# Kernel tuning notes

Measured on AMD Instinct MI355X. Metric: run time of the kernel, lower is better.

## Reference

```python
import jax, jax.numpy as jnp
import numpy as np

H = 1024      # hidden_size
F = 1024      # intermediate_size
E = 8         # num_experts
K = 2         # num_experts_per_tok
B, S = 1, 2048


def setup_inputs() -> dict:
    key = jax.random.key(0)
    ks = jax.random.split(key, 8)
    s = 0.02
    return {
        "hidden_states": jax.random.normal(ks[0], (B, S, H), jnp.float32),
        "w_gate": jax.random.normal(ks[1], (H, E), jnp.float32) * s,
        "w_gate_proj": jax.random.normal(ks[2], (E, H, F), jnp.float32) * s,   # per-expert gate_proj
        "w_up_proj": jax.random.normal(ks[3], (E, H, F), jnp.float32) * s,     # per-expert up_proj
        "w_down_proj": jax.random.normal(ks[4], (E, F, H), jnp.float32) * s,   # per-expert down_proj
        "w_shared_gate": jax.random.normal(ks[5], (H, F), jnp.float32) * s,
        "w_shared_up": jax.random.normal(ks[6], (H, F), jnp.float32) * s,
        "w_shared_down": jax.random.normal(ks[7], (F, H), jnp.float32) * s,
    }


def reference(hidden_states, w_gate, w_gate_proj, w_up_proj, w_down_proj,
              w_shared_gate, w_shared_up, w_shared_down):
    b, s, h = hidden_states.shape
    x = hidden_states.reshape(-1, h)                       # [T, H]
    t = x.shape[0]

    # --- router ---
    router_logits = x @ w_gate                             # [T, E]
    topk_vals, topk_idx = jax.lax.top_k(router_logits, K)  # [T, K]
    expert_weights = jax.nn.softmax(topk_vals.astype(jnp.float32), axis=-1).astype(x.dtype)

    # dense per-token per-expert combine weight [T, E] (zero where not selected)
    combine = jnp.zeros((t, E), x.dtype).at[jnp.arange(t)[:, None], topk_idx].add(expert_weights)

    # --- all experts as one grouped GEMM (weight-zero experts contribute 0) ---
    g = jnp.einsum('th,ehf->tef', x, w_gate_proj)          # [T, E, F]
    u = jnp.einsum('th,ehf->tef', x, w_up_proj)            # [T, E, F]
    y = jnp.einsum('tef,efh->teh', jax.nn.silu(g) * u, w_down_proj)  # [T, E, H]
    out = jnp.einsum('teh,te->th', y, combine)             # [T, H]

    # --- shared expert ---
    shared = (jax.nn.silu(x @ w_shared_gate) * (x @ w_shared_up)) @ w_shared_down
    out = (out + shared).reshape(b, s, h)

    aux_loss = jnp.float32(0.0)
    return out, aux_loss
```

## Files before the change

kernel.cpp:

```cpp
#include <hip/hip_runtime.h>
#include <hip/hip_bf16.h>
#include <stdint.h>

#define HDIM 1024
#define FDIM 1024
#define TTOK 2048
#define CAP  2048
#define MSZ  (1024*1024)

typedef __attribute__((ext_vector_type(8))) __bf16 bf16x8;
typedef __attribute__((ext_vector_type(4))) float  f32x4;

static __device__ __forceinline__ unsigned short f2bf(float v) {
  unsigned int u = __float_as_uint(v);
  u += 0x7FFF + ((u >> 16) & 1);
  return (unsigned short)(u >> 16);
}

static __device__ __forceinline__ unsigned pk2(float a, float b) {
  return (unsigned)f2bf(a) | ((unsigned)f2bf(b) << 16);
}

static __device__ __forceinline__ void gload_lds16(const void* g, void* l) {
  __builtin_amdgcn_global_load_lds(
      (const __attribute__((address_space(1))) unsigned int*)g,
      (__attribute__((address_space(3))) unsigned int*)l, 16, 0, 0);
}


__global__ __launch_bounds__(256) void k_trw(
    const float* __restrict__ wgp, const float* __restrict__ wsg,
    const float* __restrict__ wup, const float* __restrict__ wsu,
    const float* __restrict__ wdp, const float* __restrict__ wsd,
    unsigned short* __restrict__ wB) {
  int b = blockIdx.x;
  int tid = threadIdx.x;
  int m = b >> 6;
  int idx = b & 63;
  int rb = (idx >> 3) << 7;
  int cb = (idx & 7) << 7;
  const float* src;
  if (m < 8)       src = wgp + (size_t)m * MSZ;
  else if (m == 8) src = wsg;
  else if (m < 17) src = wup + (size_t)(m - 9) * MSZ;
  else if (m == 17) src = wsu;
  else if (m < 26) src = wdp + (size_t)(m - 18) * MSZ;
  else             src = wsd;
  unsigned short* dst = wB + (size_t)m * MSZ;
  __shared__ __align__(16) unsigned short T[128 * 128];
  #pragma unroll
  for (int i = 0; i < 16; i++) {
    int g = tid + (i << 8);
    int r = g >> 5;
    int f4 = g & 31;
    float4 v = *(const float4*)(src + (size_t)(rb + r) * 1024 + cb + (f4 << 2));
    uint2 p;
    p.x = pk2(v.x, v.y);
    p.y = pk2(v.z, v.w);
    int ps = (f4 + ((r >> 3) << 1)) & 31;
    *(uint2*)(T + r * 128 + (ps << 2)) = p;
  }
  __syncthreads();
  int L = tid & 63, w = tid >> 6;
  int q = L & 15;
  int cbase = (w << 2) + (L >> 4);
  #pragma unroll
  for (int j = 0; j < 8; j++) {
    int c = cbase + (j << 4);
    int ps = ((c >> 2) + (q << 1)) & 31;
    const unsigned short* p = T + (q << 3) * 128 + (ps << 2) + (c & 3);
    unsigned short u0 = p[0],       u1 = p[128],      u2 = p[2 * 128],
                   u3 = p[3 * 128], u4 = p[4 * 128],  u5 = p[5 * 128],
                   u6 = p[6 * 128], u7 = p[7 * 128];
    uint4 o;
    o.x = (unsigned)u0 | ((unsigned)u1 << 16);
    o.y = (unsigned)u2 | ((unsigned)u3 << 16);
    o.z = (unsigned)u4 | ((unsigned)u5 << 16);
    o.w = (unsigned)u6 | ((unsigned)u7 << 16);
    *(uint4*)(dst + (size_t)(cb + c) * 1024 + rb + (q << 3)) = o;
  }
}

__global__ __launch_bounds__(256) void k_rt(
    const float* __restrict__ x, const float* __restrict__ wg,
    unsigned short* __restrict__ xb,
    int* __restrict__ counts, int* __restrict__ tok_id, float* __restrict__ tok_w,
    int2* __restrict__ tsl, float* __restrict__ tw) {
  int b = blockIdx.x;
  int tid = threadIdx.x;
  if (b < 1024) {
    int i = b * 256 + tid;
    const float4* in4 = (const float4*)x;
    float4 f0 = in4[i * 2], f1 = in4[i * 2 + 1];
    uint4 v;
    v.x = pk2(f0.x, f0.y); v.y = pk2(f0.z, f0.w);
    v.z = pk2(f1.x, f1.y); v.w = pk2(f1.z, f1.w);
    *((uint4*)(xb + (size_t)i * 8)) = v;
    if (i < TTOK) { tok_id[8 * CAP + i] = i; tok_w[8 * CAP + i] = 1.0f; }
    if (i == 0) counts[8 << 4] = TTOK;
  } else {
    int t = ((b - 1024) << 2) + (tid >> 6);
    int L = tid & 63;
    const float* xr = x + (size_t)t * HDIM;
    float acc[8] = {0, 0, 0, 0, 0, 0, 0, 0};
    for (int h = L; h < HDIM; h += 64) {
      float xv = xr[h];
      const float* wr = wg + h * 8;
      #pragma unroll
      for (int e = 0; e < 8; e++) acc[e] += xv * wr[e];
    }
    #pragma unroll
    for (int e = 0; e < 8; e++) {
      float v = acc[e];
      for (int off = 32; off > 0; off >>= 1) v += __shfl_xor(v, off);
      acc[e] = v;
    }
    if (L == 0) {
      int i1 = 0; float v1 = acc[0];
      #pragma unroll
      for (int e = 1; e < 8; e++) if (acc[e] > v1) { v1 = acc[e]; i1 = e; }
      int i2 = -1; float v2 = -1e30f;
      #pragma unroll
      for (int e = 0; e < 8; e++) if (e != i1 && acc[e] > v2) { v2 = acc[e]; i2 = e; }
      float ex = __expf(v2 - v1);
      float w1 = 1.f / (1.f + ex);
      float w2 = 1.f - w1;
      int p1 = atomicAdd(&counts[i1 << 4], 1);
      tok_id[i1 * CAP + p1] = t; tok_w[i1 * CAP + p1] = w1;
      int p2 = atomicAdd(&counts[i2 << 4], 1);
      tok_id[i2 * CAP + p2] = t; tok_w[i2 * CAP + p2] = w2;
      tsl[t] = make_int2((i1 << 10) + p1, (i2 << 10) + p2);
      tw[t] = w1;
    }
  }
}


__global__ __launch_bounds__(256, 4) void k_gemm1(
    const unsigned short* __restrict__ xb, const unsigned short* __restrict__ wB,
    const int* __restrict__ counts, const int* __restrict__ tok_id,
    unsigned short* __restrict__ actb) {
  int lin = blockIdx.x;
  int e = lin >> 8;
  int r9 = lin & 255;
  int nbi = (r9 & 7) | ((r9 >> 7) << 3);
  int mi  = (r9 >> 3) & 15;
  int Ne = (e == 8) ? TTOK : counts[e << 4];
  int rb = mi << 7;
  if (rb >= Ne) return;
  int nb = nbi << 6;
  const unsigned short* wg = wB + (size_t)e * MSZ;
  const unsigned short* wu = wB + (size_t)(9 + e) * MSZ;
  __shared__ __align__(16) unsigned short As[128 * 64];
  __shared__ __align__(16) unsigned short Bgs[64 * 64];
  __shared__ __align__(16) unsigned short Bus[64 * 64];
  int tid = threadIdx.x;
  int w = tid >> 6, L = tid & 63;
  int quad = L >> 4, lane15 = L & 15;
  int wr = w >> 1, wc = w & 1;
  int l7 = lane15 & 7;
  int sw8 = ((L & 7) ^ (L >> 3)) << 3;
  const int* tlist = tok_id + e * CAP + rb;
  int trow[4];
  #pragma unroll
  for (int r = 0; r < 4; r++) {
    int row = (w << 5) + (r << 3) + (L >> 3);
    trow[r] = (rb + row < Ne) ? tlist[row] : 0;
  }
  f32x4 accg[4][2], accu[4][2];
  #pragma unroll
  for (int mt = 0; mt < 4; mt++)
    #pragma unroll
    for (int nt = 0; nt < 2; nt++) {
      accg[mt][nt] = (f32x4){0.f, 0.f, 0.f, 0.f};
      accu[mt][nt] = (f32x4){0.f, 0.f, 0.f, 0.f};
    }
  for (int it = 0; it < 16; it++) {
    int k0 = it << 6;
    #pragma unroll
    for (int r = 0; r < 4; r++)
      gload_lds16(xb + (size_t)trow[r] * 1024 + k0 + sw8, As + ((w << 2) + r) * 512);
    #pragma unroll
    for (int r = 0; r < 2; r++) {
      int fr = (((w << 1) + r) << 3) + (L >> 3);
      size_t go = (size_t)(nb + fr) * 1024 + k0 + sw8;
      gload_lds16(wg + go, Bgs + ((w << 1) + r) * 512);
      gload_lds16(wu + go, Bus + ((w << 1) + r) * 512);
    }
    __syncthreads();
    #pragma unroll
    for (int s = 0; s < 2; s++) {
      bf16x8 a[4], bg[2], bu[2];
      int ch = (s << 2) + quad;
      int po = ((ch ^ l7) << 3);
      #pragma unroll
      for (int mt = 0; mt < 4; mt++)
        a[mt] = *(const bf16x8*)(As + (((wr << 6) + (mt << 4) + lane15) << 6) + po);
      #pragma unroll
      for (int nt = 0; nt < 2; nt++) {
        int rrow = ((wc << 5) + (nt << 4) + lane15) << 6;
        bg[nt] = *(const bf16x8*)(Bgs + rrow + po);
        bu[nt] = *(const bf16x8*)(Bus + rrow + po);
      }
      #pragma unroll
      for (int mt = 0; mt < 4; mt++)
        #pragma unroll
        for (int nt = 0; nt < 2; nt++) {
          accg[mt][nt] = __builtin_amdgcn_mfma_f32_16x16x32_bf16(a[mt], bg[nt], accg[mt][nt], 0, 0, 0);
          accu[mt][nt] = __builtin_amdgcn_mfma_f32_16x16x32_bf16(a[mt], bu[nt], accu[mt][nt], 0, 0, 0);
        }
    }
    __syncthreads();
  }
  #pragma unroll
  for (int mt = 0; mt < 4; mt++)
    #pragma unroll
    for (int nt = 0; nt < 2; nt++)
      #pragma unroll
      for (int g = 0; g < 4; g++) {
        int r = (wr << 6) + (mt << 4) + (quad << 2) + g;
        if (rb + r < Ne) {
          float gv = accg[mt][nt][g], uv = accu[mt][nt][g];
          float av = gv / (1.f + __expf(-gv)) * uv;
          int f = nb + (wc << 5) + (nt << 4) + lane15;
          actb[(size_t)(e * CAP + rb + r) * 1024 + f] = f2bf(av);
        }
      }
}

__global__ __launch_bounds__(256, 4) void k_gemm2(
    const unsigned short* __restrict__ actb, const unsigned short* __restrict__ wB,
    const int* __restrict__ counts, float* __restrict__ y) {
  int lin = blockIdx.x;
  int e = lin >> 8;
  int r8 = lin & 255;
  int nbi = r8 & 7;
  int mi  = r8 >> 3;
  int Ne = (e == 8) ? TTOK : counts[e << 4];
  int rb = mi << 6;
  if (rb >= Ne) return;
  int nb = nbi << 7;
  int yb = (e < 8) ? (e << 10) : 8192;
  const unsigned short* wd = wB + (size_t)(18 + e) * MSZ;
  __shared__ __align__(16) unsigned short As[64 * 64];
  __shared__ __align__(16) unsigned short Bs[128 * 64];
  int tid = threadIdx.x;
  int w = tid >> 6, L = tid & 63;
  int quad = L >> 4, lane15 = L & 15;
  int l7 = lane15 & 7;
  int sw8 = ((L & 7) ^ (L >> 3)) << 3;
  const unsigned short* arow = actb + (size_t)(e * CAP + rb) * 1024;
  f32x4 acc[4][2];
  #pragma unroll
  for (int mt = 0; mt < 4; mt++)
    #pragma unroll
    for (int nt = 0; nt < 2; nt++) acc[mt][nt] = (f32x4){0.f, 0.f, 0.f, 0.f};
  for (int it = 0; it < 16; it++) {
    int k0 = it << 6;
    #pragma unroll
    for (int r = 0; r < 2; r++) {
      int row = (w << 4) + (r << 3) + (L >> 3);
      gload_lds16(arow + (size_t)row * 1024 + k0 + sw8, As + ((w << 1) + r) * 512);
    }
    #pragma unroll
    for (int r = 0; r < 4; r++) {
      int row = (w << 5) + (r << 3) + (L >> 3);
      gload_lds16(wd + (size_t)(nb + row) * 1024 + k0 + sw8, Bs + ((w << 2) + r) * 512);
    }
    __syncthreads();
    #pragma unroll
    for (int s = 0; s < 2; s++) {
      bf16x8 a[4], b[2];
      int ch = (s << 2) + quad;
      int po = ((ch ^ l7) << 3);
      #pragma unroll
      for (int mt = 0; mt < 4; mt++)
        a[mt] = *(const bf16x8*)(As + (((mt << 4) + lane15) << 6) + po);
      #pragma unroll
      for (int nt = 0; nt < 2; nt++)
        b[nt] = *(const bf16x8*)(Bs + (((w << 5) + (nt << 4) + lane15) << 6) + po);
      #pragma unroll
      for (int mt = 0; mt < 4; mt++)
        #pragma unroll
        for (int nt = 0; nt < 2; nt++)
          acc[mt][nt] = __builtin_amdgcn_mfma_f32_16x16x32_bf16(a[mt], b[nt], acc[mt][nt], 0, 0, 0);
    }
    __syncthreads();
  }
  #pragma unroll
  for (int mt = 0; mt < 4; mt++)
    #pragma unroll
    for (int nt = 0; nt < 2; nt++)
      #pragma unroll
      for (int g = 0; g < 4; g++) {
        int r = (mt << 4) + (quad << 2) + g;
        if (rb + r < Ne) {
          int hc = nb + (w << 5) + (nt << 4) + lane15;
          y[(size_t)(yb + rb + r) * 1024 + hc] = acc[mt][nt][g];
        }
      }
}

__global__ __launch_bounds__(256) void k_comb(
    const float* __restrict__ y, const int2* __restrict__ tsl,
    const float* __restrict__ tw, float* __restrict__ out) {
  int t = blockIdx.x, tid = threadIdx.x;
  int2 s = tsl[t];
  float w0 = tw[t], w1 = 1.f - w0;
  const float4* y4 = (const float4*)y;
  float4 a = y4[(size_t)s.x * 256 + tid];
  float4 b = y4[(size_t)s.y * 256 + tid];
  float4 c = y4[(size_t)(8192 + t) * 256 + tid];
  float4 o;
  o.x = w0 * a.x + w1 * b.x + c.x;
  o.y = w0 * a.y + w1 * b.y + c.y;
  o.z = w0 * a.z + w1 * b.z + c.z;
  o.w = w0 * a.w + w1 * b.w + c.w;
  ((float4*)out)[(size_t)t * 256 + tid] = o;
}

extern "C" void kernel_launch(void* const* d_in, const int* in_sizes, int n_in,
                              void* d_out, int out_size, void* d_ws, size_t ws_size,
                              hipStream_t stream) {
  (void)in_sizes; (void)n_in; (void)ws_size; (void)out_size;
  const float* x   = (const float*)d_in[0];
  const float* wg  = (const float*)d_in[1];
  const float* wgp = (const float*)d_in[2];
  const float* wup = (const float*)d_in[3];
  const float* wdp = (const float*)d_in[4];
  const float* wsg = (const float*)d_in[5];
  const float* wsu = (const float*)d_in[6];
  const float* wsd = (const float*)d_in[7];
  float* out = (float*)d_out;
  char* ws = (char*)d_ws;
  unsigned short* wB   = (unsigned short*)ws;
  unsigned short* xb   = (unsigned short*)(ws + 56623104);
  unsigned short* actb = (unsigned short*)(ws + 60817408);
  float* y      = (float*)(ws + 98566144);
  int*   tok_id = (int*)(ws + 140509184);
  float* tok_w  = (float*)(ws + 140582912);
  int2*  tsl    = (int2*)(ws + 140656640);
  float* tw     = (float*)(ws + 140673024);
  int*   counts = (int*)(ws + 140681216);

  hipMemsetAsync(counts, 0, 576, stream);
  k_trw<<<1728, 256, 0, stream>>>(wgp, wsg, wup, wsu, wdp, wsd, wB);
  k_rt<<<1536, 256, 0, stream>>>(x, wg, xb, counts, tok_id, tok_w, tsl, tw);
  k_gemm1<<<2304, 256, 0, stream>>>(xb, wB, counts, tok_id, actb);
  k_gemm2<<<2304, 256, 0, stream>>>(actb, wB, counts, y);
  k_comb<<<2048, 256, 0, stream>>>(y, tsl, tw, out);
}
```

Before: 263.4 us.

## Double-buffer LDS tiles in expert GEMMs and merge prep kernels into one launch

Both grouped GEMM kernels now use two LDS buffers, so the next K-tile's global-to-LDS loads are issued before the current tile's MFMA compute, giving one barrier per tile instead of two. The weight transpose/convert kernel and the router/activation-convert kernel are merged into a single launch, which removes one kernel launch and lets the two kinds of work run side by side. The larger LDS footprint lowers the occupancy hints to 2 and 3 blocks per CU, which reduces latency hiding from other waves.

```diff
diff --git a/kernel.cpp b/kernel.cpp
--- a/kernel.cpp
+++ b/kernel.cpp
@@ -28,78 +28,18 @@
 }
 
 
-__global__ __launch_bounds__(256) void k_trw(
+__global__ __launch_bounds__(256) void k_prep(
+    const float* __restrict__ x, const float* __restrict__ wg,
     const float* __restrict__ wgp, const float* __restrict__ wsg,
     const float* __restrict__ wup, const float* __restrict__ wsu,
     const float* __restrict__ wdp, const float* __restrict__ wsd,
-    unsigned short* __restrict__ wB) {
-  int b = blockIdx.x;
-  int tid = threadIdx.x;
-  int m = b >> 6;
-  int idx = b & 63;
-  int rb = (idx >> 3) << 7;
-  int cb = (idx & 7) << 7;
-  const float* src;
-  if (m < 8)       src = wgp + (size_t)m * MSZ;
-  else if (m == 8) src = wsg;
-  else if (m < 17) src = wup + (size_t)(m - 9) * MSZ;
-  else if (m == 17) src = wsu;
-  else if (m < 26) src = wdp + (size_t)(m - 18) * MSZ;
-  else             src = wsd;
-  unsigned short* dst = wB + (size_t)m * MSZ;
-  __shared__ __align__(16) unsigned short T[128 * 128];
-  #pragma unroll
-  for (int i = 0; i < 16; i++) {
-    int g = tid + (i << 8);
-    int r = g >> 5;
-    int f4 = g & 31;
-    float4 v = *(const float4*)(src + (size_t)(rb + r) * 1024 + cb + (f4 << 2));
-    uint2 p;
-    p.x = pk2(v.x, v.y);
-    p.y = pk2(v.z, v.w);
-    int ps = (f4 + ((r >> 3) << 1)) & 31;
-    *(uint2*)(T + r * 128 + (ps << 2)) = p;
-  }
-  __syncthreads();
-  int L = tid & 63, w = tid >> 6;
-  int q = L & 15;
-  int cbase = (w << 2) + (L >> 4);
-  #pragma unroll
-  for (int j = 0; j < 8; j++) {
-    int c = cbase + (j << 4);
-    int ps = ((c >> 2) + (q << 1)) & 31;
-    const unsigned short* p = T + (q << 3) * 128 + (ps << 2) + (c & 3);
-    unsigned short u0 = p[0],       u1 = p[128],      u2 = p[2 * 128],
-                   u3 = p[3 * 128], u4 = p[4 * 128],  u5 = p[5 * 128],
-                   u6 = p[6 * 128], u7 = p[7 * 128];
-    uint4 o;
-    o.x = (unsigned)u0 | ((unsigned)u1 << 16);
-    o.y = (unsigned)u2 | ((unsigned)u3 << 16);
-    o.z = (unsigned)u4 | ((unsigned)u5 << 16);
-    o.w = (unsigned)u6 | ((unsigned)u7 << 16);
-    *(uint4*)(dst + (size_t)(cb + c) * 1024 + rb + (q << 3)) = o;
-  }
-}
-
-__global__ __launch_bounds__(256) void k_rt(
-    const float* __restrict__ x, const float* __restrict__ wg,
-    unsigned short* __restrict__ xb,
+    unsigned short* __restrict__ wB, unsigned short* __restrict__ xb,
     int* __restrict__ counts, int* __restrict__ tok_id, float* __restrict__ tok_w,
     int2* __restrict__ tsl, float* __restrict__ tw) {
   int b = blockIdx.x;
   int tid = threadIdx.x;
-  if (b < 1024) {
-    int i = b * 256 + tid;
-    const float4* in4 = (const float4*)x;
-    float4 f0 = in4[i * 2], f1 = in4[i * 2 + 1];
-    uint4 v;
-    v.x = pk2(f0.x, f0.y); v.y = pk2(f0.z, f0.w);
-    v.z = pk2(f1.x, f1.y); v.w = pk2(f1.z, f1.w);
-    *((uint4*)(xb + (size_t)i * 8)) = v;
-    if (i < TTOK) { tok_id[8 * CAP + i] = i; tok_w[8 * CAP + i] = 1.0f; }
-    if (i == 0) counts[8 << 4] = TTOK;
-  } else {
-    int t = ((b - 1024) << 2) + (tid >> 6);
+  if (b < 512) {
+    int t = (b << 2) + (tid >> 6);
     int L = tid & 63;
     const float* xr = x + (size_t)t * HDIM;
     float acc[8] = {0, 0, 0, 0, 0, 0, 0, 0};
@@ -132,11 +72,67 @@
       tsl[t] = make_int2((i1 << 10) + p1, (i2 << 10) + p2);
       tw[t] = w1;
     }
+  } else if (b < 1536) {
+    int i = (b - 512) * 256 + tid;
+    const float4* in4 = (const float4*)x;
+    float4 f0 = in4[i * 2], f1 = in4[i * 2 + 1];
+    uint4 v;
+    v.x = pk2(f0.x, f0.y); v.y = pk2(f0.z, f0.w);
+    v.z = pk2(f1.x, f1.y); v.w = pk2(f1.z, f1.w);
+    *((uint4*)(xb + (size_t)i * 8)) = v;
+    if (i < TTOK) { tok_id[8 * CAP + i] = i; tok_w[8 * CAP + i] = 1.0f; }
+    if (i == 0) counts[8 << 4] = TTOK;
+  } else {
+    int bt = b - 1536;
+    int m = bt >> 6;
+    int idx = bt & 63;
+    int rb = (idx >> 3) << 7;
+    int cb = (idx & 7) << 7;
+    const float* src;
+    if (m < 8)       src = wgp + (size_t)m * MSZ;
+    else if (m == 8) src = wsg;
+    else if (m < 17) src = wup + (size_t)(m - 9) * MSZ;
+    else if (m == 17) src = wsu;
+    else if (m < 26) src = wdp + (size_t)(m - 18) * MSZ;
+    else             src = wsd;
+    unsigned short* dst = wB + (size_t)m * MSZ;
+    __shared__ __align__(16) unsigned short T[128 * 128];
+    #pragma unroll
+    for (int i = 0; i < 16; i++) {
+      int g = tid + (i << 8);
+      int r = g >> 5;
+      int f4 = g & 31;
+      float4 v = *(const float4*)(src + (size_t)(rb + r) * 1024 + cb + (f4 << 2));
+      uint2 p;
+      p.x = pk2(v.x, v.y);
+      p.y = pk2(v.z, v.w);
+      int ps = (f4 + ((r >> 3) << 1)) & 31;
+      *(uint2*)(T + r * 128 + (ps << 2)) = p;
+    }
+    __syncthreads();
+    int L = tid & 63, w = tid >> 6;
+    int q = L & 15;
+    int cbase = (w << 2) + (L >> 4);
+    #pragma unroll
+    for (int j = 0; j < 8; j++) {
+      int c = cbase + (j << 4);
+      int ps = ((c >> 2) + (q << 1)) & 31;
+      const unsigned short* p = T + (q << 3) * 128 + (ps << 2) + (c & 3);
+      unsigned short u0 = p[0],       u1 = p[128],      u2 = p[2 * 128],
+                     u3 = p[3 * 128], u4 = p[4 * 128],  u5 = p[5 * 128],
+                     u6 = p[6 * 128], u7 = p[7 * 128];
+      uint4 o;
+      o.x = (unsigned)u0 | ((unsigned)u1 << 16);
+      o.y = (unsigned)u2 | ((unsigned)u3 << 16);
+      o.z = (unsigned)u4 | ((unsigned)u5 << 16);
+      o.w = (unsigned)u6 | ((unsigned)u7 << 16);
+      *(uint4*)(dst + (size_t)(cb + c) * 1024 + rb + (q << 3)) = o;
+    }
   }
 }
 
 
-__global__ __launch_bounds__(256, 4) void k_gemm1(
+__global__ __launch_bounds__(256, 2) void k_gemm1(
     const unsigned short* __restrict__ xb, const unsigned short* __restrict__ wB,
     const int* __restrict__ counts, const int* __restrict__ tok_id,
     unsigned short* __restrict__ actb) {
@@ -151,9 +147,12 @@
   int nb = nbi << 6;
   const unsigned short* wg = wB + (size_t)e * MSZ;
   const unsigned short* wu = wB + (size_t)(9 + e) * MSZ;
-  __shared__ __align__(16) unsigned short As[128 * 64];
-  __shared__ __align__(16) unsigned short Bgs[64 * 64];
-  __shared__ __align__(16) unsigned short Bus[64 * 64];
+  __shared__ __align__(16) unsigned short As0[128 * 64];
+  __shared__ __align__(16) unsigned short As1[128 * 64];
+  __shared__ __align__(16) unsigned short Bg0[64 * 64];
+  __shared__ __align__(16) unsigned short Bg1[64 * 64];
+  __shared__ __align__(16) unsigned short Bu0[64 * 64];
+  __shared__ __align__(16) unsigned short Bu1[64 * 64];
   int tid = threadIdx.x;
   int w = tid >> 6, L = tid & 63;
   int quad = L >> 4, lane15 = L & 15;
@@ -175,19 +174,22 @@
       accg[mt][nt] = (f32x4){0.f, 0.f, 0.f, 0.f};
       accu[mt][nt] = (f32x4){0.f, 0.f, 0.f, 0.f};
     }
-  for (int it = 0; it < 16; it++) {
+  auto stage = [&](unsigned short* As_, unsigned short* Bg_, unsigned short* Bu_,
+                   int it) {
     int k0 = it << 6;
     #pragma unroll
     for (int r = 0; r < 4; r++)
-      gload_lds16(xb + (size_t)trow[r] * 1024 + k0 + sw8, As + ((w << 2) + r) * 512);
+      gload_lds16(xb + (size_t)trow[r] * 1024 + k0 + sw8, As_ + ((w << 2) + r) * 512);
     #pragma unroll
     for (int r = 0; r < 2; r++) {
       int fr = (((w << 1) + r) << 3) + (L >> 3);
       size_t go = (size_t)(nb + fr) * 1024 + k0 + sw8;
-      gload_lds16(wg + go, Bgs + ((w << 1) + r) * 512);
-      gload_lds16(wu + go, Bus + ((w << 1) + r) * 512);
-    }
-    __syncthreads();
+      gload_lds16(wg + go, Bg_ + ((w << 1) + r) * 512);
+      gload_lds16(wu + go, Bu_ + ((w << 1) + r) * 512);
+    }
+  };
+  auto compute = [&](const unsigned short* As_, const unsigned short* Bg_,
+                     const unsigned short* Bu_) {
     #pragma unroll
     for (int s = 0; s < 2; s++) {
       bf16x8 a[4], bg[2], bu[2];
@@ -195,12 +197,12 @@
       int po = ((ch ^ l7) << 3);
       #pragma unroll
       for (int mt = 0; mt < 4; mt++)
-        a[mt] = *(const bf16x8*)(As + (((wr << 6) + (mt << 4) + lane15) << 6) + po);
+        a[mt] = *(const bf16x8*)(As_ + (((wr << 6) + (mt << 4) + lane15) << 6) + po);
       #pragma unroll
       for (int nt = 0; nt < 2; nt++) {
         int rrow = ((wc << 5) + (nt << 4) + lane15) << 6;
-        bg[nt] = *(const bf16x8*)(Bgs + rrow + po);
-        bu[nt] = *(const bf16x8*)(Bus + rrow + po);
+        bg[nt] = *(const bf16x8*)(Bg_ + rrow + po);
+        bu[nt] = *(const bf16x8*)(Bu_ + rrow + po);
       }
       #pragma unroll
       for (int mt = 0; mt < 4; mt++)
@@ -210,6 +212,16 @@
           accu[mt][nt] = __builtin_amdgcn_mfma_f32_16x16x32_bf16(a[mt], bu[nt], accu[mt][nt], 0, 0, 0);
         }
     }
+  };
+  stage(As0, Bg0, Bu0, 0);
+  __syncthreads();
+  for (int it2 = 0; it2 < 8; it2++) {
+    int itA = it2 << 1;
+    if (itA + 1 < 16) stage(As1, Bg1, Bu1, itA + 1);
+    compute(As0, Bg0, Bu0);
+    __syncthreads();
+    if (itA + 2 < 16) stage(As0, Bg0, Bu0, itA + 2);
+    compute(As1, Bg1, Bu1);
     __syncthreads();
   }
   #pragma unroll
@@ -228,7 +240,7 @@
       }
 }
 
-__global__ __launch_bounds__(256, 4) void k_gemm2(
+__global__ __launch_bounds__(256, 3) void k_gemm2(
     const unsigned short* __restrict__ actb, const unsigned short* __restrict__ wB,
     const int* __restrict__ counts, float* __restrict__ y) {
   int lin = blockIdx.x;
@@ -242,8 +254,10 @@
   int nb = nbi << 7;
   int yb = (e < 8) ? (e << 10) : 8192;
   const unsigned short* wd = wB + (size_t)(18 + e) * MSZ;
-  __shared__ __align__(16) unsigned short As[64 * 64];
-  __shared__ __align__(16) unsigned short Bs[128 * 64];
+  __shared__ __align__(16) unsigned short As0[64 * 64];
+  __shared__ __align__(16) unsigned short As1[64 * 64];
+  __shared__ __align__(16) unsigned short Bs0[128 * 64];
+  __shared__ __align__(16) unsigned short Bs1[128 * 64];
   int tid = threadIdx.x;
   int w = tid >> 6, L = tid & 63;
   int quad = L >> 4, lane15 = L & 15;
@@ -255,19 +269,20 @@
   for (int mt = 0; mt < 4; mt++)
     #pragma unroll
     for (int nt = 0; nt < 2; nt++) acc[mt][nt] = (f32x4){0.f, 0.f, 0.f, 0.f};
-  for (int it = 0; it < 16; it++) {
+  auto stage = [&](unsigned short* As_, unsigned short* Bs_, int it) {
     int k0 = it << 6;
     #pragma unroll
     for (int r = 0; r < 2; r++) {
       int row = (w << 4) + (r << 3) + (L >> 3);
-      gload_lds16(arow + (size_t)row * 1024 + k0 + sw8, As + ((w << 1) + r) * 512);
+      gload_lds16(arow + (size_t)row * 1024 + k0 + sw8, As_ + ((w << 1) + r) * 512);
     }
     #pragma unroll
     for (int r = 0; r < 4; r++) {
       int row = (w << 5) + (r << 3) + (L >> 3);
-      gload_lds16(wd + (size_t)(nb + row) * 1024 + k0 + sw8, Bs + ((w << 2) + r) * 512);
-    }
-    __syncthreads();
+      gload_lds16(wd + (size_t)(nb + row) * 1024 + k0 + sw8, Bs_ + ((w << 2) + r) * 512);
+    }
+  };
+  auto compute = [&](const unsigned short* As_, const unsigned short* Bs_) {
     #pragma unroll
     for (int s = 0; s < 2; s++) {
       bf16x8 a[4], b[2];
@@ -275,16 +290,26 @@
       int po = ((ch ^ l7) << 3);
       #pragma unroll
       for (int mt = 0; mt < 4; mt++)
-        a[mt] = *(const bf16x8*)(As + (((mt << 4) + lane15) << 6) + po);
+        a[mt] = *(const bf16x8*)(As_ + (((mt << 4) + lane15) << 6) + po);
       #pragma unroll
       for (int nt = 0; nt < 2; nt++)
-        b[nt] = *(const bf16x8*)(Bs + (((w << 5) + (nt << 4) + lane15) << 6) + po);
+        b[nt] = *(const bf16x8*)(Bs_ + (((w << 5) + (nt << 4) + lane15) << 6) + po);
       #pragma unroll
       for (int mt = 0; mt < 4; mt++)
         #pragma unroll
         for (int nt = 0; nt < 2; nt++)
           acc[mt][nt] = __builtin_amdgcn_mfma_f32_16x16x32_bf16(a[mt], b[nt], acc[mt][nt], 0, 0, 0);
     }
+  };
+  stage(As0, Bs0, 0);
+  __syncthreads();
+  for (int it2 = 0; it2 < 8; it2++) {
+    int itA = it2 << 1;
+    if (itA + 1 < 16) stage(As1, Bs1, itA + 1);
+    compute(As0, Bs0);
+    __syncthreads();
+    if (itA + 2 < 16) stage(As0, Bs0, itA + 2);
+    compute(As1, Bs1);
     __syncthreads();
   }
   #pragma unroll
@@ -344,8 +369,8 @@
   int*   counts = (int*)(ws + 140681216);
 
   hipMemsetAsync(counts, 0, 576, stream);
-  k_trw<<<1728, 256, 0, stream>>>(wgp, wsg, wup, wsu, wdp, wsd, wB);
-  k_rt<<<1536, 256, 0, stream>>>(x, wg, xb, counts, tok_id, tok_w, tsl, tw);
+  k_prep<<<3264, 256, 0, stream>>>(x, wg, wgp, wsg, wup, wsu, wdp, wsd,
+                                   wB, xb, counts, tok_id, tok_w, tsl, tw);
   k_gemm1<<<2304, 256, 0, stream>>>(xb, wB, counts, tok_id, actb);
   k_gemm2<<<2304, 256, 0, stream>>>(actb, wB, counts, y);
   k_comb<<<2048, 256, 0, stream>>>(y, tsl, tw, out);
```

Result: faster. 243.5 us (-7.5%).
